# Kernel tuning notes

Hardware: AMD Instinct MI355X
Metric: run time of the kernel (lower is better)

## Reference

```python
import jax, jax.numpy as jnp
import numpy as np

V, E, H, Z = 32000, 256, 512, 64
B, T = 32, 128
PAD = 0


def _n(k, shape, s=0.05):
    return jax.random.normal(k, shape, jnp.float32) * s


def setup_inputs() -> dict:
    key = jax.random.key(0)
    ks = jax.random.split(key, 32)
    inp = {
        "x": jax.random.randint(ks[0], (B, T), 0, V),
        "y": jax.random.randint(ks[1], (B, T), 0, V),
        "epsilon": jax.random.normal(ks[2], (Z,), jnp.float32),
        "enc_emb": _n(ks[3], (V, E)).at[PAD].set(0.0),  # padding_idx row zeroed
        "dec_emb": _n(ks[4], (V, E)),
        "fwd_Wih": _n(ks[5], (4 * H, E)), "fwd_Whh": _n(ks[6], (4 * H, H)), "fwd_b": _n(ks[7], (4 * H,)),
        "bwd_Wih": _n(ks[8], (4 * H, E)), "bwd_Whh": _n(ks[9], (4 * H, H)), "bwd_b": _n(ks[10], (4 * H,)),
        "dec_Wih": _n(ks[11], (4 * H, E)), "dec_Whh": _n(ks[12], (4 * H, H)), "dec_b": _n(ks[13], (4 * H,)),
        "enc_hW": _n(ks[14], (H, 2 * H)), "enc_hb": _n(ks[15], (H,)),
        "mu_W": _n(ks[16], (Z, H)), "mu_b": _n(ks[17], (Z,)),
        "std_W": _n(ks[18], (Z, H)), "std_b": _n(ks[19], (Z,)),
        "dec_hW": _n(ks[20], (H, Z)), "dec_hb": _n(ks[21], (H,)),
        "out_W": _n(ks[22], (V, H)), "out_b": _n(ks[23], (V,)),
    }
    return inp


def lstm_scan(e, h0, c0, Wih, Whh, b):
    # e: [B,T,E]; returns all hidden states [B,T,H] and final (h,c)
    def step(carry, x_t):
        h, c = carry
        g = x_t @ Wih.T + h @ Whh.T + b  # [B,4H], torch gate order i,f,g,o
        i, f, gg, o = jnp.split(g, 4, axis=-1)
        c = jax.nn.sigmoid(f) * c + jax.nn.sigmoid(i) * jnp.tanh(gg)
        h = jax.nn.sigmoid(o) * jnp.tanh(c)
        return (h, c), h
    (hT, cT), hs = jax.lax.scan(step, (h0, c0), jnp.swapaxes(e, 0, 1))
    return jnp.swapaxes(hs, 0, 1), hT, cT


def reference(x, y, epsilon, enc_emb, dec_emb,
              fwd_Wih, fwd_Whh, fwd_b, bwd_Wih, bwd_Whh, bwd_b,
              dec_Wih, dec_Whh, dec_b, enc_hW, enc_hb,
              mu_W, mu_b, std_W, std_b, dec_hW, dec_hb, out_W, out_b):
    Bx = x.shape[0]
    zeros = jnp.zeros((Bx, H), jnp.float32)
    # ---- encoder: two unidirectional LSTMs (second over flipped seq) ----
    ef = enc_emb[x]                 # [B,T,E]
    eb = enc_emb[x[:, ::-1]]
    _, hf, _ = lstm_scan(ef, zeros, zeros, fwd_Wih, fwd_Whh, fwd_b)
    _, hb, _ = lstm_scan(eb, zeros, zeros, bwd_Wih, bwd_Whh, bwd_b)
    h = jnp.concatenate([hf, hb], axis=1) @ enc_hW.T + enc_hb  # [B,H] (no activation)
    mu = h @ mu_W.T + mu_b
    sigma = jax.nn.softplus(h @ std_W.T + std_b)
    # ---- reparameterization (single epsilon shared across batch, as in torch) ----
    z = mu + sigma * epsilon        # [B,Z]
    # ---- decoder ----
    h0 = jnp.tanh(z @ dec_hW.T + dec_hb)  # [B,H]
    ed = dec_emb[x]
    hs, _, _ = lstm_scan(ed, h0, jnp.zeros_like(h0), dec_Wih, dec_Whh, dec_b)  # [B,T,H]
    logits = hs @ out_W.T + out_b   # [B,T,V]
    # ---- losses ----
    logp = jax.nn.log_softmax(logits.reshape(-1, V), axis=-1)
    ce = -jnp.take_along_axis(logp, y.reshape(-1, 1), axis=1).sum()
    kl = -0.5 * (1.0 + jnp.log(sigma) - mu ** 2 - sigma).sum()
    return (kl + ce) / Bx
```

## Files before the change

kernel.cpp:

```cpp
#include <hip/hip_runtime.h>
#include <hip/hip_bf16.h>

typedef float f32x4 __attribute__((ext_vector_type(4)));
typedef short s16x8 __attribute__((ext_vector_type(8)));
typedef unsigned int u32;
typedef unsigned short u16;

#define DEV static __device__ __forceinline__

namespace {
constexpr int V = 32000, E = 256, H = 512, Z = 64, B = 32, T = 128;
constexpr u32 POISON = 0xFFFFFFFFu;
constexpr int GUARD = 1 << 20;

constexpr size_t OFF_ZF   = 0;
constexpr size_t OFF_ZB   = 32768;
constexpr size_t OFF_PF   = 65536;
constexpr size_t OFF_PB   = OFF_PF + (size_t)T * 32768;
constexpr size_t OFF_H0   = OFF_PB + (size_t)T * 32768;
constexpr size_t OFF_HENC = OFF_H0 + 32768;
constexpr size_t OFF_HS   = OFF_HENC + 32768;
constexpr size_t OFF_LGY  = OFF_HS + (size_t)B*T*H*2;
constexpr size_t OFF_CER  = OFF_LGY + 16384;
constexpr size_t OFF_PEND = OFF_CER + 16384;
constexpr size_t OFF_Z    = OFF_PEND;
constexpr size_t OFF_KLP  = OFF_Z + 8192;
constexpr size_t OFF_WB   = OFF_KLP + 256;
constexpr size_t OFF_CEP  = OFF_PF;
}

DEV u16 f2b(float f) {
  u32 x = __builtin_bit_cast(u32, f);
  return (u16)((x + 0x7fffu + ((x >> 16) & 1u)) >> 16);
}
DEV float b2f(u16 u) {
  u32 x = ((u32)u) << 16;
  return __builtin_bit_cast(float, x);
}
DEV float fsig(float x) { return 1.f / (1.f + __expf(-x)); }
DEV float ftanh(float x) { return 2.f / (1.f + __expf(-2.f * x)) - 1.f; }

DEV u32 aload(const u32* p) { return __hip_atomic_load(p, __ATOMIC_RELAXED, __HIP_MEMORY_SCOPE_AGENT); }
DEV void astore(u32* p, u32 v) { __hip_atomic_store(p, v, __ATOMIC_RELAXED, __HIP_MEMORY_SCOPE_AGENT); }
DEV void afstore(u32* p, float v) { astore(p, __builtin_bit_cast(u32, v)); }

DEV u32* hslot(char* ws, int dir, int s) {
  size_t off = (s == 0) ? (dir ? OFF_ZB : OFF_ZF)
                        : ((dir ? OFF_PB : OFF_PF) + (size_t)(s - 1) * 32768);
  return reinterpret_cast<u32*>(ws + off);
}

__global__ __launch_bounds__(512, 1) void phaseA_k(
    const int* __restrict__ x, const float* __restrict__ emb,
    const float* __restrict__ fWih, const float* __restrict__ fWhh, const float* __restrict__ fb,
    const float* __restrict__ bWih, const float* __restrict__ bWhh, const float* __restrict__ bb,
    const float* __restrict__ enc_hW, const float* __restrict__ enc_hb,
    const float* __restrict__ mu_W, const float* __restrict__ mu_b,
    const float* __restrict__ std_W, const float* __restrict__ std_b,
    const float* __restrict__ epsv, const float* __restrict__ out_W,
    char* __restrict__ ws)
{
  __shared__ __align__(16) u16 Wl[64][776];
  __shared__ __align__(16) u16 act[32][776];
  __shared__ __align__(16) float gates[64][33];

  const int tid = threadIdx.x;
  const int wg = blockIdx.x;

  if (wg >= 64) {
    const size_t total = (size_t)V * H / 8;
    for (size_t idx = (size_t)(wg - 64) * 512 + tid; idx < total; idx += (size_t)128 * 512) {
      const float4* src = reinterpret_cast<const float4*>(out_W + idx * 8);
      float4 a = src[0], b = src[1];
      s16x8 o;
      o[0] = (short)f2b(a.x); o[1] = (short)f2b(a.y); o[2] = (short)f2b(a.z); o[3] = (short)f2b(a.w);
      o[4] = (short)f2b(b.x); o[5] = (short)f2b(b.y); o[6] = (short)f2b(b.z); o[7] = (short)f2b(b.w);
      *reinterpret_cast<s16x8*>(ws + OFF_WB + idx * 16) = o;
    }
    return;
  }

  const bool bwd = wg >= 32;
  const int dir = bwd ? 1 : 0;
  const int lw = wg & 31;
  const int u0 = lw * 16;
  const float* Wih = bwd ? bWih : fWih;
  const float* Whh = bwd ? bWhh : fWhh;
  const float* bv  = bwd ? bb : fb;

  {
    int r = tid >> 3, s8 = tid & 7;
    int grow = (r >> 4) * H + u0 + (r & 15);
    for (int kc = s8 * 96; kc < s8 * 96 + 96; kc += 8) {
      const float4* p;
      if (kc < E) p = reinterpret_cast<const float4*>(Wih + (size_t)grow * E + kc);
      else        p = reinterpret_cast<const float4*>(Whh + (size_t)grow * H + (kc - E));
      float4 a = p[0], b4 = p[1];
      Wl[r][kc+0] = f2b(a.x);  Wl[r][kc+1] = f2b(a.y);  Wl[r][kc+2] = f2b(a.z);  Wl[r][kc+3] = f2b(a.w);
      Wl[r][kc+4] = f2b(b4.x); Wl[r][kc+5] = f2b(b4.y); Wl[r][kc+6] = f2b(b4.z); Wl[r][kc+7] = f2b(b4.w);
    }
  }

  const int ab = tid >> 4, au = tid & 15;
  const float Bi = bv[0*H + u0 + au], Bf = bv[1*H + u0 + au];
  const float Bg = bv[2*H + u0 + au], Bo = bv[3*H + u0 + au];
  float c = 0.f;

  const int wv = tid >> 6, lane = tid & 63, l15 = lane & 15, lhi = lane >> 4;
  const int mq = wv & 3, nh = wv >> 2;
  u32* actu = reinterpret_cast<u32*>(&act[0][0]);

  auto stage_emb = [&](int t) {
    int tt = bwd ? (T - 1 - t) : t;
    const float* src = emb + (size_t)x[ab * T + tt] * E + au * 16;
    const float4* s4 = reinterpret_cast<const float4*>(src);
    float4 A0 = s4[0], A1 = s4[1], A2 = s4[2], A3 = s4[3];
    u32 w0 = f2b(A0.x) | ((u32)f2b(A0.y) << 16);
    u32 w1 = f2b(A0.z) | ((u32)f2b(A0.w) << 16);
    u32 w2 = f2b(A1.x) | ((u32)f2b(A1.y) << 16);
    u32 w3 = f2b(A1.z) | ((u32)f2b(A1.w) << 16);
    u32 w4 = f2b(A2.x) | ((u32)f2b(A2.y) << 16);
    u32 w5 = f2b(A2.z) | ((u32)f2b(A2.w) << 16);
    u32 w6 = f2b(A3.x) | ((u32)f2b(A3.y) << 16);
    u32 w7 = f2b(A3.z) | ((u32)f2b(A3.w) << 16);
    u32* dst = actu + ab * 388 + au * 8;
    reinterpret_cast<uint4*>(dst)[0] = make_uint4(w0, w1, w2, w3);
    reinterpret_cast<uint4*>(dst)[1] = make_uint4(w4, w5, w6, w7);
  };

  stage_emb(0);

  for (int t = 0; t < T; ++t) {
    {
      const u32* hsrc = hslot(ws, dir, t);
      u32 tmp[16];
      #pragma unroll
      for (int j = 0; j < 16; ++j) tmp[j] = aload(hsrc + tid + j * 512);
      int guard = 0;
      while (true) {
        bool bad = false;
        #pragma unroll
        for (int j = 0; j < 16; ++j)
          if (tmp[j] == POISON) { bad = true; tmp[j] = aload(hsrc + tid + j * 512); }
        if (!bad || ++guard > GUARD) break;
        __builtin_amdgcn_s_sleep(1);
      }
      #pragma unroll
      for (int j = 0; j < 16; ++j) {
        int i = tid + j * 512;
        actu[(i >> 8) * 388 + 128 + (i & 255)] = tmp[j];
      }
    }
    __syncthreads();

    {
      f32x4 ac0 = {0,0,0,0}, ac1 = {0,0,0,0}, ac2 = {0,0,0,0}, ac3 = {0,0,0,0};
      #pragma unroll
      for (int s = 0; s < 6; ++s) {
        int kk = s * 128 + lhi * 8;
        s16x8 A0 = *reinterpret_cast<const s16x8*>(&Wl[mq * 16 + l15][kk]);
        s16x8 B0 = *reinterpret_cast<const s16x8*>(&act[nh * 16 + l15][kk]);
        ac0 = __builtin_amdgcn_mfma_f32_16x16x32_bf16(A0, B0, ac0, 0, 0, 0);
        s16x8 A1 = *reinterpret_cast<const s16x8*>(&Wl[mq * 16 + l15][kk + 32]);
        s16x8 B1 = *reinterpret_cast<const s16x8*>(&act[nh * 16 + l15][kk + 32]);
        ac1 = __builtin_amdgcn_mfma_f32_16x16x32_bf16(A1, B1, ac1, 0, 0, 0);
        s16x8 A2 = *reinterpret_cast<const s16x8*>(&Wl[mq * 16 + l15][kk + 64]);
        s16x8 B2 = *reinterpret_cast<const s16x8*>(&act[nh * 16 + l15][kk + 64]);
        ac2 = __builtin_amdgcn_mfma_f32_16x16x32_bf16(A2, B2, ac2, 0, 0, 0);
        s16x8 A3 = *reinterpret_cast<const s16x8*>(&Wl[mq * 16 + l15][kk + 96]);
        s16x8 B3 = *reinterpret_cast<const s16x8*>(&act[nh * 16 + l15][kk + 96]);
        ac3 = __builtin_amdgcn_mfma_f32_16x16x32_bf16(A3, B3, ac3, 0, 0, 0);
      }
      #pragma unroll
      for (int reg = 0; reg < 4; ++reg)
        gates[mq * 16 + lhi * 4 + reg][nh * 16 + l15] =
            (ac0[reg] + ac1[reg]) + (ac2[reg] + ac3[reg]);
    }
    __syncthreads();

    {
      float gi = gates[ 0 + au][ab] + Bi;
      float gf = gates[16 + au][ab] + Bf;
      float gg = gates[32 + au][ab] + Bg;
      float go = gates[48 + au][ab] + Bo;
      c = fsig(gf) * c + fsig(gi) * ftanh(gg);
      float h = fsig(go) * ftanh(c);
      u32 bits = f2b(h);
      u32 other = (u32)__shfl_down((int)bits, 1);
      if ((au & 1) == 0) {
        u32* dst = hslot(ws, dir, t + 1) + ab * 256 + (u0 + au) / 2;
        astore(dst, bits | (other << 16));
      }
    }
    __syncthreads();
    if (t != T - 1) stage_emb(t + 1);
  }

  {
    u32* wlu = reinterpret_cast<u32*>(&Wl[0][0]);
    const u32* hf = hslot(ws, 0, T);
    const u32* hb = hslot(ws, 1, T);
    u32 tmp[32];
    #pragma unroll
    for (int j = 0; j < 32; ++j) {
      int i = tid + j * 512, b = i >> 9, k = i & 511;
      tmp[j] = (k < 256) ? aload(hf + b * 256 + k) : aload(hb + b * 256 + (k - 256));
    }
    int guard = 0;
    while (true) {
      bool bad = false;
      #pragma unroll
      for (int j = 0; j < 32; ++j)
        if (tmp[j] == POISON) {
          bad = true;
          int i = tid + j * 512, b = i >> 9, k = i & 511;
          tmp[j] = (k < 256) ? aload(hf + b * 256 + k) : aload(hb + b * 256 + (k - 256));
        }
      if (!bad || ++guard > GUARD) break;
      __builtin_amdgcn_s_sleep(1);
    }
    #pragma unroll
    for (int j = 0; j < 32; ++j) wlu[tid + j * 512] = tmp[j];
  }
  __syncthreads();
  if (tid < 256) {
    const u16* hcat = &Wl[0][0];
    int b = tid >> 3, jc = tid & 7;
    int j = wg * 8 + jc;
    float s = enc_hb[j];
    const float4* w4 = reinterpret_cast<const float4*>(enc_hW + (size_t)j * 1024);
    for (int kk = 0; kk < 256; ++kk) {
      float4 wv4 = w4[kk];
      const u16* hp = hcat + b * 1024 + kk * 4;
      s += wv4.x * b2f(hp[0]) + wv4.y * b2f(hp[1]) + wv4.z * b2f(hp[2]) + wv4.w * b2f(hp[3]);
    }
    u32 bits = f2b(s);
    u32 other = (u32)__shfl_down((int)bits, 1);
    if ((jc & 1) == 0) {
      u32* dst = reinterpret_cast<u32*>(ws + OFF_HENC) + b * 256 + j / 2;
      astore(dst, bits | (other << 16));
    }
  }
  __syncthreads();

  {
    u32* hhu = reinterpret_cast<u32*>(&act[0][0]);
    const u32* he = reinterpret_cast<const u32*>(ws + OFF_HENC);
    u32 tmp[16];
    #pragma unroll
    for (int j = 0; j < 16; ++j) tmp[j] = aload(he + tid + j * 512);
    int guard = 0;
    while (true) {
      bool bad = false;
      #pragma unroll
      for (int j = 0; j < 16; ++j)
        if (tmp[j] == POISON) { bad = true; tmp[j] = aload(he + tid + j * 512); }
      if (!bad || ++guard > GUARD) break;
      __builtin_amdgcn_s_sleep(1);
    }
    #pragma unroll
    for (int j = 0; j < 16; ++j) hhu[tid + j * 512] = tmp[j];
  }
  __syncthreads();
  {
    const u16* hh = &act[0][0];
    int b = tid >> 4, l16 = tid & 15;
    float pm = 0.f, ps = 0.f;
    const float* mwr = mu_W + (size_t)wg * H;
    const float* swr = std_W + (size_t)wg * H;
    for (int k = l16 * 32; k < l16 * 32 + 32; ++k) {
      float hv = b2f(hh[b * H + k]);
      pm += mwr[k] * hv;
      ps += swr[k] * hv;
    }
    gates[b][l16] = pm;
    gates[32 + b][l16] = ps;
  }
  __syncthreads();
  if (tid < 32) {
    int b = tid;
    float mu = mu_b[wg], sv = std_b[wg];
    for (int l = 0; l < 16; ++l) { mu += gates[b][l]; sv += gates[32 + b][l]; }
    float sig = fmaxf(sv, 0.f) + log1pf(__expf(-fabsf(sv)));
    float zv = mu + sig * epsv[wg];
    reinterpret_cast<float*>(ws + OFF_Z)[b * Z + wg] = zv;
    gates[b][16] = -0.5f * (1.f + logf(sig) - mu * mu - sig);
  }
  __syncthreads();
  if (tid == 0) {
    float kl = 0.f;
    for (int b = 0; b < 32; ++b) kl += gates[b][16];
    reinterpret_cast<float*>(ws + OFF_KLP)[wg] = kl;
  }
}

__global__ __launch_bounds__(512, 1) void phaseB_k(
    const int* __restrict__ x, const int* __restrict__ y,
    const float* __restrict__ emb,
    const float* __restrict__ Wih, const float* __restrict__ Whh, const float* __restrict__ bv,
    const float* __restrict__ dec_hW, const float* __restrict__ dec_hb,
    const float* __restrict__ out_W, const float* __restrict__ out_b,
    char* __restrict__ ws, float* __restrict__ out)
{
  __shared__ __align__(16) char smem[157440];
  const int tid = threadIdx.x;
  const int bid = blockIdx.x;
  u32* hsu = reinterpret_cast<u32*>(ws + OFF_HS);
  const int wid = tid >> 6, lane = tid & 63, l15 = lane & 15, lhi = lane >> 4;

  if (bid < 32) {
    u16 (*Wl)[776]  = reinterpret_cast<u16(*)[776]>(smem);
    u16 (*act)[776] = reinterpret_cast<u16(*)[776]>(smem + 99328);
    float (*gates)[33] = reinterpret_cast<float(*)[33]>(smem + 148992);
    const int wg = bid;
    const int u0 = wg * 16;

    {
      int r = tid >> 3, s8 = tid & 7;
      int grow = (r >> 4) * H + u0 + (r & 15);
      for (int kc = s8 * 96; kc < s8 * 96 + 96; kc += 8) {
        const float4* p;
        if (kc < E) p = reinterpret_cast<const float4*>(Wih + (size_t)grow * E + kc);
        else        p = reinterpret_cast<const float4*>(Whh + (size_t)grow * H + (kc - E));
        float4 a = p[0], b4 = p[1];
        Wl[r][kc+0] = f2b(a.x);  Wl[r][kc+1] = f2b(a.y);  Wl[r][kc+2] = f2b(a.z);  Wl[r][kc+3] = f2b(a.w);
        Wl[r][kc+4] = f2b(b4.x); Wl[r][kc+5] = f2b(b4.y); Wl[r][kc+6] = f2b(b4.z); Wl[r][kc+7] = f2b(b4.w);
      }
    }

    const int ab = tid >> 4, au = tid & 15;
    const float Bi = bv[0*H + u0 + au], Bf = bv[1*H + u0 + au];
    const float Bg = bv[2*H + u0 + au], Bo = bv[3*H + u0 + au];
    float c = 0.f;

    u32* h0u = reinterpret_cast<u32*>(ws + OFF_H0);
    const float* zws = reinterpret_cast<const float*>(ws + OFF_Z);
    u32* actu = reinterpret_cast<u32*>(&act[0][0]);
    const int mq = wid & 3, nh = wid >> 2;

    auto stage_emb = [&](int t) {
      const float* src = emb + (size_t)x[ab * T + t] * E + au * 16;
      const float4* s4 = reinterpret_cast<const float4*>(src);
      float4 A0 = s4[0], A1 = s4[1], A2 = s4[2], A3 = s4[3];
      u32 w0 = f2b(A0.x) | ((u32)f2b(A0.y) << 16);
      u32 w1 = f2b(A0.z) | ((u32)f2b(A0.w) << 16);
      u32 w2 = f2b(A1.x) | ((u32)f2b(A1.y) << 16);
      u32 w3 = f2b(A1.z) | ((u32)f2b(A1.w) << 16);
      u32 w4 = f2b(A2.x) | ((u32)f2b(A2.y) << 16);
      u32 w5 = f2b(A2.z) | ((u32)f2b(A2.w) << 16);
      u32 w6 = f2b(A3.x) | ((u32)f2b(A3.y) << 16);
      u32 w7 = f2b(A3.z) | ((u32)f2b(A3.w) << 16);
      u32* dst = actu + ab * 388 + au * 8;
      reinterpret_cast<uint4*>(dst)[0] = make_uint4(w0, w1, w2, w3);
      reinterpret_cast<uint4*>(dst)[1] = make_uint4(w4, w5, w6, w7);
    };

    stage_emb(0);

    {
      float s = dec_hb[u0 + au];
      const float* wr = dec_hW + (size_t)(u0 + au) * Z;
      for (int zz = 0; zz < Z; ++zz) s += wr[zz] * zws[ab * Z + zz];
      float h0 = ftanh(s);
      u32 bits = f2b(h0);
      u32 other = (u32)__shfl_down((int)bits, 1);
      if ((au & 1) == 0) astore(h0u + ab * 256 + (u0 + au) / 2, bits | (other << 16));
    }

    for (int t = 0; t < T; ++t) {
      {
        u32 tmp[16];
        const u32* base = (t == 0) ? h0u : (hsu + (size_t)(t - 1) * B * 256);
        #pragma unroll
        for (int j = 0; j < 16; ++j) tmp[j] = aload(base + tid + j * 512);
        int guard = 0;
        while (true) {
          bool bad = false;
          #pragma unroll
          for (int j = 0; j < 16; ++j)
            if (tmp[j] == POISON) { bad = true; tmp[j] = aload(base + tid + j * 512); }
          if (!bad || ++guard > GUARD) break;
          __builtin_amdgcn_s_sleep(1);
        }
        #pragma unroll
        for (int j = 0; j < 16; ++j) {
          int i = tid + j * 512;
          actu[(i >> 8) * 388 + 128 + (i & 255)] = tmp[j];
        }
      }
      __syncthreads();

      {
        f32x4 ac0 = {0,0,0,0}, ac1 = {0,0,0,0}, ac2 = {0,0,0,0}, ac3 = {0,0,0,0};
        #pragma unroll
        for (int s = 0; s < 6; ++s) {
          int kk = s * 128 + lhi * 8;
          s16x8 A0 = *reinterpret_cast<const s16x8*>(&Wl[mq * 16 + l15][kk]);
          s16x8 B0 = *reinterpret_cast<const s16x8*>(&act[nh * 16 + l15][kk]);
          ac0 = __builtin_amdgcn_mfma_f32_16x16x32_bf16(A0, B0, ac0, 0, 0, 0);
          s16x8 A1 = *reinterpret_cast<const s16x8*>(&Wl[mq * 16 + l15][kk + 32]);
          s16x8 B1 = *reinterpret_cast<const s16x8*>(&act[nh * 16 + l15][kk + 32]);
          ac1 = __builtin_amdgcn_mfma_f32_16x16x32_bf16(A1, B1, ac1, 0, 0, 0);
          s16x8 A2 = *reinterpret_cast<const s16x8*>(&Wl[mq * 16 + l15][kk + 64]);
          s16x8 B2 = *reinterpret_cast<const s16x8*>(&act[nh * 16 + l15][kk + 64]);
          ac2 = __builtin_amdgcn_mfma_f32_16x16x32_bf16(A2, B2, ac2, 0, 0, 0);
          s16x8 A3 = *reinterpret_cast<const s16x8*>(&Wl[mq * 16 + l15][kk + 96]);
          s16x8 B3 = *reinterpret_cast<const s16x8*>(&act[nh * 16 + l15][kk + 96]);
          ac3 = __builtin_amdgcn_mfma_f32_16x16x32_bf16(A3, B3, ac3, 0, 0, 0);
        }
        #pragma unroll
        for (int reg = 0; reg < 4; ++reg)
          gates[mq * 16 + lhi * 4 + reg][nh * 16 + l15] =
              (ac0[reg] + ac1[reg]) + (ac2[reg] + ac3[reg]);
      }
      __syncthreads();

      {
        float gi = gates[ 0 + au][ab] + Bi;
        float gf = gates[16 + au][ab] + Bf;
        float gg = gates[32 + au][ab] + Bg;
        float go = gates[48 + au][ab] + Bo;
        c = fsig(gf) * c + fsig(gi) * ftanh(gg);
        float h = fsig(go) * ftanh(c);
        u32 bits = f2b(h);
        u32 other = (u32)__shfl_down((int)bits, 1);
        if ((au & 1) == 0) {
          u32* dst = hsu + (size_t)(t * B + ab) * 256 + (u0 + au) / 2;
          astore(dst, bits | (other << 16));
        }
      }
      __syncthreads();
      if (t != T - 1) stage_emb(t + 1);
    }
    return;
  }

  const int w = bid - 32;
  u16 (*At)[72] = reinterpret_cast<u16(*)[72]>(smem);
  u16 (*Bt)[72] = reinterpret_cast<u16(*)[72]>(smem + 18432);
  float* red = reinterpret_cast<float*>(smem + 55296);
  const u16* Wb = reinterpret_cast<const u16*>(ws + OFF_WB);
  const int wm = wid & 1, wn = wid >> 1;
  const int sr = tid >> 3, ss = tid & 7;

  for (int tl = w; tl < 4000; tl += 192) {
    const int rt = tl / 125, ct = tl % 125;
    const int row0 = rt * 128, col0 = ct * 256;

    f32x4 acc[4][4];
    #pragma unroll
    for (int i = 0; i < 4; ++i)
      #pragma unroll
      for (int j = 0; j < 4; ++j) acc[i][j] = {0, 0, 0, 0};

    for (int kt = 0; kt < 8; ++kt) {
      #pragma unroll
      for (int it = 0; it < 2; ++it) {
        int r = it * 64 + sr;
        const u32* p = hsu + (size_t)(row0 + r) * 256 + kt * 32 + ss * 4;
        u32 a0 = aload(p), a1 = aload(p + 1), a2 = aload(p + 2), a3 = aload(p + 3);
        int guard = 0;
        while ((a0 == POISON || a1 == POISON || a2 == POISON || a3 == POISON) && ++guard <= GUARD) {
          __builtin_amdgcn_s_sleep(64);
          a0 = aload(p); a1 = aload(p + 1); a2 = aload(p + 2); a3 = aload(p + 3);
        }
        u32* d = reinterpret_cast<u32*>(&At[r][ss * 8]);
        d[0] = a0; d[1] = a1; d[2] = a2; d[3] = a3;
      }
      #pragma unroll
      for (int it = 0; it < 4; ++it) {
        int r = it * 64 + sr;
        *reinterpret_cast<s16x8*>(&Bt[r][ss * 8]) =
            *reinterpret_cast<const s16x8*>(Wb + (size_t)(col0 + r) * H + kt * 64 + ss * 8);
      }
      __syncthreads();
      #pragma unroll
      for (int ks = 0; ks < 2; ++ks) {
        int kk = ks * 32 + lhi * 8;
        s16x8 af[4], bf[4];
        #pragma unroll
        for (int mi = 0; mi < 4; ++mi)
          af[mi] = *reinterpret_cast<const s16x8*>(&At[wm * 64 + mi * 16 + l15][kk]);
        #pragma unroll
        for (int ni = 0; ni < 4; ++ni)
          bf[ni] = *reinterpret_cast<const s16x8*>(&Bt[wn * 64 + ni * 16 + l15][kk]);
        #pragma unroll
        for (int mi = 0; mi < 4; ++mi)
          #pragma unroll
          for (int ni = 0; ni < 4; ++ni)
            acc[mi][ni] = __builtin_amdgcn_mfma_f32_16x16x32_bf16(af[mi], bf[ni], acc[mi][ni], 0, 0, 0);
      }
      __syncthreads();
    }

    float bias[4];
    #pragma unroll
    for (int ni = 0; ni < 4; ++ni) bias[ni] = out_b[col0 + wn * 64 + ni * 16 + l15];

    #pragma unroll
    for (int mi = 0; mi < 4; ++mi) {
      #pragma unroll
      for (int reg = 0; reg < 4; ++reg) {
        float l0 = acc[mi][0][reg] + bias[0];
        float l1 = acc[mi][1][reg] + bias[1];
        float l2 = acc[mi][2][reg] + bias[2];
        float l3 = acc[mi][3][reg] + bias[3];
        float m = fmaxf(fmaxf(l0, l1), fmaxf(l2, l3));
        for (int d = 1; d < 16; d <<= 1) m = fmaxf(m, __shfl_xor(m, d, 16));
        float s = __expf(l0 - m) + __expf(l1 - m) + __expf(l2 - m) + __expf(l3 - m);
        for (int d = 1; d < 16; d <<= 1) s += __shfl_xor(s, d, 16);
        if (l15 == 0) {
          int lr = mi * 16 + lhi * 4 + reg;
          red[((wm * 64 + lr) * 4 + wn) * 2 + 0] = m;
          red[((wm * 64 + lr) * 4 + wn) * 2 + 1] = s;
        }
      }
    }
    __syncthreads();
    if (tid < 128) {
      int lr = tid;
      float M = -3.0e38f, S = 0.f;
      #pragma unroll
      for (int wnn = 0; wnn < 4; ++wnn) {
        float m = red[(lr * 4 + wnn) * 2 + 0];
        float s = red[(lr * 4 + wnn) * 2 + 1];
        float nm = fmaxf(M, m);
        S = S * __expf(M - nm) + s * __expf(m - nm);
        M = nm;
      }
      u32* cepw = reinterpret_cast<u32*>(ws + OFF_CEP);
      size_t ix = ((size_t)ct * 4096 + row0 + lr) * 2;
      afstore(cepw + ix + 0, M);
      afstore(cepw + ix + 1, S);
    }
    __syncthreads();
  }

  for (int r = w * 8 + wid; r < 4096; r += 192 * 8) {
    int t = r >> 5, b = r & 31;
    int yy = y[b * T + t];
    const u32* hp = hsu + (size_t)r * 256 + lane * 4;
    u32 a0 = aload(hp), a1 = aload(hp + 1), a2 = aload(hp + 2), a3 = aload(hp + 3);
    int guard = 0;
    while ((a0 == POISON || a1 == POISON || a2 == POISON || a3 == POISON) && ++guard <= GUARD) {
      __builtin_amdgcn_s_sleep(64);
      a0 = aload(hp); a1 = aload(hp + 1); a2 = aload(hp + 2); a3 = aload(hp + 3);
    }
    const float4* wp = reinterpret_cast<const float4*>(out_W + (size_t)yy * H + lane * 8);
    float4 w0 = wp[0], w1 = wp[1];
    float s = b2f((u16)(a0 & 0xFFFF)) * w0.x + b2f((u16)(a0 >> 16)) * w0.y
            + b2f((u16)(a1 & 0xFFFF)) * w0.z + b2f((u16)(a1 >> 16)) * w0.w
            + b2f((u16)(a2 & 0xFFFF)) * w1.x + b2f((u16)(a2 >> 16)) * w1.y
            + b2f((u16)(a3 & 0xFFFF)) * w1.z + b2f((u16)(a3 >> 16)) * w1.w;
    for (int d = 1; d < 64; d <<= 1) s += __shfl_xor(s, d);
    if (lane == 0)
      afstore(reinterpret_cast<u32*>(ws + OFF_LGY) + r, s + out_b[yy]);
  }

  {
    int r = w * 512 + tid;
    if (r < 4096) {
      const u32* lgyu = reinterpret_cast<const u32*>(ws + OFF_LGY);
      u32 lb = aload(lgyu + r);
      int guard = 0;
      while (lb == POISON && ++guard <= GUARD) { __builtin_amdgcn_s_sleep(64); lb = aload(lgyu + r); }
      float ly = __builtin_bit_cast(float, lb);
      const u32* cp = reinterpret_cast<const u32*>(ws + OFF_CEP);
      float M = -3.0e38f, S = 0.f;
      for (int cch = 0; cch < 125; ++cch) {
        size_t ix = ((size_t)cch * 4096 + r) * 2;
        u32 ma = aload(cp + ix), sa = aload(cp + ix + 1);
        int g2 = 0;
        while ((ma == POISON || sa == POISON) && ++g2 <= GUARD) {
          __builtin_amdgcn_s_sleep(64);
          ma = aload(cp + ix); sa = aload(cp + ix + 1);
        }
        float m = __builtin_bit_cast(float, ma), s = __builtin_bit_cast(float, sa);
        float nm = fmaxf(M, m);
        S = S * __expf(M - nm) + s * __expf(m - nm);
        M = nm;
      }
      afstore(reinterpret_cast<u32*>(ws + OFF_CER) + r, M + logf(S) - ly);
    }
  }

  if (w == 0) {
    __syncthreads();
    float* rb = reinterpret_cast<float*>(smem);
    const u32* ceru = reinterpret_cast<const u32*>(ws + OFF_CER);
    const float* klp = reinterpret_cast<const float*>(ws + OFF_KLP);
    float s = 0.f;
    for (int j = 0; j < 8; ++j) {
      int r = tid + j * 512;
      u32 v = aload(ceru + r);
      int guard = 0;
      while (v == POISON && ++guard <= GUARD) { __builtin_amdgcn_s_sleep(64); v = aload(ceru + r); }
      s += __builtin_bit_cast(float, v);
    }
    if (tid < 64) s += klp[tid];
    rb[tid] = s;
    __syncthreads();
    for (int d = 256; d > 0; d >>= 1) {
      if (tid < d) rb[tid] += rb[tid + d];
      __syncthreads();
    }
    if (tid == 0) out[0] = rb[0] / 32.f;
  }
}

extern "C" void kernel_launch(void* const* d_in, const int* in_sizes, int n_in,
                              void* d_out, int out_size, void* d_ws, size_t ws_size,
                              hipStream_t stream) {
  (void)in_sizes; (void)n_in; (void)out_size; (void)ws_size;
  const int*   x       = (const int*)d_in[0];
  const int*   y       = (const int*)d_in[1];
  const float* epsv    = (const float*)d_in[2];
  const float* enc_emb = (const float*)d_in[3];
  const float* dec_emb = (const float*)d_in[4];
  const float* fWih    = (const float*)d_in[5];
  const float* fWhh    = (const float*)d_in[6];
  const float* fb      = (const float*)d_in[7];
  const float* bWih    = (const float*)d_in[8];
  const float* bWhh    = (const float*)d_in[9];
  const float* bb      = (const float*)d_in[10];
  const float* dWih    = (const float*)d_in[11];
  const float* dWhh    = (const float*)d_in[12];
  const float* db      = (const float*)d_in[13];
  const float* enc_hW  = (const float*)d_in[14];
  const float* enc_hb  = (const float*)d_in[15];
  const float* mu_W    = (const float*)d_in[16];
  const float* mu_b    = (const float*)d_in[17];
  const float* std_W   = (const float*)d_in[18];
  const float* std_b   = (const float*)d_in[19];
  const float* dec_hW  = (const float*)d_in[20];
  const float* dec_hb  = (const float*)d_in[21];
  const float* out_W   = (const float*)d_in[22];
  const float* out_b   = (const float*)d_in[23];
  char* ws = (char*)d_ws;

  hipMemsetAsync(ws + OFF_ZF, 0x00, 65536, stream);
  hipMemsetAsync(ws + OFF_PF, 0xFF, OFF_PEND - OFF_PF, stream);

  phaseA_k<<<192, 512, 0, stream>>>(x, enc_emb, fWih, fWhh, fb, bWih, bWhh, bb,
                                    enc_hW, enc_hb, mu_W, mu_b, std_W, std_b,
                                    epsv, out_W, ws);

  hipMemsetAsync(ws + OFF_CEP, 0xFF, 4096000, stream);

  phaseB_k<<<224, 512, 0, stream>>>(x, y, dec_emb, dWih, dWhh, db, dec_hW, dec_hb,
                                    out_W, out_b, ws, (float*)d_out);
}
```

Before: 1.133 ms.

## Interleave gate rows so LSTM cell update runs directly on MFMA accumulators

The per-workgroup weight tile is reordered so that the four gates (i,f,g,o) of one hidden unit land in the four accumulator registers of one MFMA lane. The cell update then runs straight from registers, which removes the shared-memory gates buffer and one __syncthreads per timestep in both the encoder and decoder recurrences. The h pairing shuffle now spans 16 lanes instead of 1. Separately, the cross-entropy partial (max,sum) buffer is transposed to row-major per row, so the final reduction reads contiguous chunks per thread, while the producing tiles now write strided.

```diff
diff --git a/kernel.cpp b/kernel.cpp
--- a/kernel.cpp
+++ b/kernel.cpp
@@ -90,7 +90,7 @@
 
   {
     int r = tid >> 3, s8 = tid & 7;
-    int grow = (r >> 4) * H + u0 + (r & 15);
+    int grow = (r & 3) * H + u0 + (r >> 2);
     for (int kc = s8 * 96; kc < s8 * 96 + 96; kc += 8) {
       const float4* p;
       if (kc < E) p = reinterpret_cast<const float4*>(Wih + (size_t)grow * E + kc);
@@ -102,12 +102,13 @@
   }
 
   const int ab = tid >> 4, au = tid & 15;
-  const float Bi = bv[0*H + u0 + au], Bf = bv[1*H + u0 + au];
-  const float Bg = bv[2*H + u0 + au], Bo = bv[3*H + u0 + au];
-  float c = 0.f;
-
   const int wv = tid >> 6, lane = tid & 63, l15 = lane & 15, lhi = lane >> 4;
   const int mq = wv & 3, nh = wv >> 2;
+  const int unit = u0 + mq * 4 + lhi;
+  const int batch = nh * 16 + l15;
+  const float Bi = bv[0*H + unit], Bf = bv[1*H + unit];
+  const float Bg = bv[2*H + unit], Bo = bv[3*H + unit];
+  float c = 0.f;
   u32* actu = reinterpret_cast<u32*>(&act[0][0]);
 
   auto stage_emb = [&](int t) {
@@ -171,24 +172,14 @@
         s16x8 B3 = *reinterpret_cast<const s16x8*>(&act[nh * 16 + l15][kk + 96]);
         ac3 = __builtin_amdgcn_mfma_f32_16x16x32_bf16(A3, B3, ac3, 0, 0, 0);
       }
-      #pragma unroll
-      for (int reg = 0; reg < 4; ++reg)
-        gates[mq * 16 + lhi * 4 + reg][nh * 16 + l15] =
-            (ac0[reg] + ac1[reg]) + (ac2[reg] + ac3[reg]);
-    }
-    __syncthreads();
-
-    {
-      float gi = gates[ 0 + au][ab] + Bi;
-      float gf = gates[16 + au][ab] + Bf;
-      float gg = gates[32 + au][ab] + Bg;
-      float go = gates[48 + au][ab] + Bo;
+      f32x4 ac = (ac0 + ac1) + (ac2 + ac3);
+      float gi = ac[0] + Bi, gf = ac[1] + Bf, gg = ac[2] + Bg, go = ac[3] + Bo;
       c = fsig(gf) * c + fsig(gi) * ftanh(gg);
       float h = fsig(go) * ftanh(c);
       u32 bits = f2b(h);
-      u32 other = (u32)__shfl_down((int)bits, 1);
-      if ((au & 1) == 0) {
-        u32* dst = hslot(ws, dir, t + 1) + ab * 256 + (u0 + au) / 2;
+      u32 other = (u32)__shfl_down((int)bits, 16);
+      if ((lhi & 1) == 0) {
+        u32* dst = hslot(ws, dir, t + 1) + batch * 256 + (unit >> 1);
         astore(dst, bits | (other << 16));
       }
     }
@@ -311,13 +302,12 @@
   if (bid < 32) {
     u16 (*Wl)[776]  = reinterpret_cast<u16(*)[776]>(smem);
     u16 (*act)[776] = reinterpret_cast<u16(*)[776]>(smem + 99328);
-    float (*gates)[33] = reinterpret_cast<float(*)[33]>(smem + 148992);
     const int wg = bid;
     const int u0 = wg * 16;
 
     {
       int r = tid >> 3, s8 = tid & 7;
-      int grow = (r >> 4) * H + u0 + (r & 15);
+      int grow = (r & 3) * H + u0 + (r >> 2);
       for (int kc = s8 * 96; kc < s8 * 96 + 96; kc += 8) {
         const float4* p;
         if (kc < E) p = reinterpret_cast<const float4*>(Wih + (size_t)grow * E + kc);
@@ -329,14 +319,16 @@
     }
 
     const int ab = tid >> 4, au = tid & 15;
-    const float Bi = bv[0*H + u0 + au], Bf = bv[1*H + u0 + au];
-    const float Bg = bv[2*H + u0 + au], Bo = bv[3*H + u0 + au];
+    const int mq = wid & 3, nh = wid >> 2;
+    const int unit = u0 + mq * 4 + lhi;
+    const int batch = nh * 16 + l15;
+    const float Bi = bv[0*H + unit], Bf = bv[1*H + unit];
+    const float Bg = bv[2*H + unit], Bo = bv[3*H + unit];
     float c = 0.f;
 
     u32* h0u = reinterpret_cast<u32*>(ws + OFF_H0);
     const float* zws = reinterpret_cast<const float*>(ws + OFF_Z);
     u32* actu = reinterpret_cast<u32*>(&act[0][0]);
-    const int mq = wid & 3, nh = wid >> 2;
 
     auto stage_emb = [&](int t) {
       const float* src = emb + (size_t)x[ab * T + t] * E + au * 16;
@@ -408,24 +400,14 @@
           s16x8 B3 = *reinterpret_cast<const s16x8*>(&act[nh * 16 + l15][kk + 96]);
           ac3 = __builtin_amdgcn_mfma_f32_16x16x32_bf16(A3, B3, ac3, 0, 0, 0);
         }
-        #pragma unroll
-        for (int reg = 0; reg < 4; ++reg)
-          gates[mq * 16 + lhi * 4 + reg][nh * 16 + l15] =
-              (ac0[reg] + ac1[reg]) + (ac2[reg] + ac3[reg]);
-      }
-      __syncthreads();
-
-      {
-        float gi = gates[ 0 + au][ab] + Bi;
-        float gf = gates[16 + au][ab] + Bf;
-        float gg = gates[32 + au][ab] + Bg;
-        float go = gates[48 + au][ab] + Bo;
+        f32x4 ac = (ac0 + ac1) + (ac2 + ac3);
+        float gi = ac[0] + Bi, gf = ac[1] + Bf, gg = ac[2] + Bg, go = ac[3] + Bo;
         c = fsig(gf) * c + fsig(gi) * ftanh(gg);
         float h = fsig(go) * ftanh(c);
         u32 bits = f2b(h);
-        u32 other = (u32)__shfl_down((int)bits, 1);
-        if ((au & 1) == 0) {
-          u32* dst = hsu + (size_t)(t * B + ab) * 256 + (u0 + au) / 2;
+        u32 other = (u32)__shfl_down((int)bits, 16);
+        if ((lhi & 1) == 0) {
+          u32* dst = hsu + (size_t)(t * B + batch) * 256 + (unit >> 1);
           astore(dst, bits | (other << 16));
         }
       }
@@ -529,7 +511,7 @@
         M = nm;
       }
       u32* cepw = reinterpret_cast<u32*>(ws + OFF_CEP);
-      size_t ix = ((size_t)ct * 4096 + row0 + lr) * 2;
+      size_t ix = ((size_t)(row0 + lr) * 125 + ct) * 2;
       afstore(cepw + ix + 0, M);
       afstore(cepw + ix + 1, S);
     }
@@ -568,7 +550,7 @@
       const u32* cp = reinterpret_cast<const u32*>(ws + OFF_CEP);
       float M = -3.0e38f, S = 0.f;
       for (int cch = 0; cch < 125; ++cch) {
-        size_t ix = ((size_t)cch * 4096 + r) * 2;
+        size_t ix = ((size_t)r * 125 + cch) * 2;
         u32 ma = aload(cp + ix), sa = aload(cp + ix + 1);
         int g2 = 0;
         while ((ma == POISON || sa == POISON) && ++g2 <= GUARD) {
```

After: 1.165 ms. +2.9%, slower.
